# Optimization experiments

Hardware: AMD Instinct MI355X
Metric: run time of the kernel (lower is better)

## Reference

```python
import jax, jax.numpy as jnp
import numpy as np

ALPHA = 1.5
TEMPERATURE = 1.0
N_ITER = 25
N_EMBED = 2048
NUM_EXPERTS = 64
N_TOKENS = 32768


def entmax_bisect(X, alpha=ALPHA, n_iter=N_ITER):
    """Faithful port of entmax.entmax_bisect forward (dim=-1)."""
    d = X.shape[-1]
    inv = 1.0 / (alpha - 1.0)
    Xa = X * (alpha - 1.0)
    max_val = jnp.max(Xa, axis=-1, keepdims=True)
    # _gp(1, alpha) = 1 ; _gp(1/d, alpha) = (1/d)**(1/(alpha-1))
    tau_lo = max_val - 1.0
    tau_hi = max_val - (1.0 / d) ** inv

    def p(tau):
        return jnp.clip(Xa - tau, 0.0, None) ** inv

    f_lo = jnp.sum(p(tau_lo), axis=-1, keepdims=True) - 1.0
    dm0 = tau_hi - tau_lo

    def body(carry, _):
        tau_lo, dm = carry
        dm = dm * 0.5
        tau_m = tau_lo + dm
        p_m = p(tau_m)
        f_m = jnp.sum(p_m, axis=-1, keepdims=True) - 1.0
        mask = (f_m * f_lo) >= 0
        tau_lo = jnp.where(mask, tau_m, tau_lo)
        return (tau_lo, dm), tau_m

    (tau_lo, dm), tau_ms = jax.lax.scan(body, (tau_lo, dm0), None, length=n_iter)
    tau_m_last = tau_ms[-1]  # [..., 1] tau used for the returned p_m in torch loop
    p_m = p(tau_m_last)
    # ensure_sum_one
    p_m = p_m / jnp.sum(p_m, axis=-1, keepdims=True)
    return p_m


def setup_inputs() -> dict:
    key = jax.random.key(0)
    kx, kw, kb = jax.random.split(key, 3)
    x = jax.random.normal(kx, (N_TOKENS, N_EMBED), dtype=jnp.float32)
    # nn.Linear default init: U(-1/sqrt(fan_in), 1/sqrt(fan_in))
    bound = 1.0 / np.sqrt(N_EMBED)
    W = jax.random.uniform(kw, (NUM_EXPERTS, N_EMBED), dtype=jnp.float32, minval=-bound, maxval=bound)
    b = jax.random.uniform(kb, (NUM_EXPERTS,), dtype=jnp.float32, minval=-bound, maxval=bound)
    return {"x": x, "W": W, "b": b}


def reference(x, W, b):
    logits = jnp.einsum("td,ed->te", x, W) + b  # [T, E]
    scaled_logits = logits / TEMPERATURE
    return entmax_bisect(scaled_logits)
```

## Files before the change

kernel.cpp:

```cpp
#include <hip/hip_runtime.h>
#include <hip/hip_bf16.h>
#include <stdint.h>

typedef __bf16 bf16x8 __attribute__((ext_vector_type(8)));
typedef float  f32x4  __attribute__((ext_vector_type(4)));

#define N_EMBED   2048
#define N_EXP     64
#define KCHUNK    64
#define NKC       (N_EMBED / KCHUNK)
#define GCH       16
#define TILEB     16384
#define LGT_STRIDE 68
#define LGT_FLOATS (64 * LGT_STRIDE)

__global__ __launch_bounds__(256) void convert_w_kernel(
        const float* __restrict__ W, uint8_t* __restrict__ wsimg) {
    int tid = blockIdx.x * 256 + threadIdx.x;
    int e   = tid >> 8;
    int d0  = (tid & 255) * 8;
    int kc  = d0 >> 6;
    int dd0 = d0 & 63;
    const float* src = W + e * N_EMBED + d0;
    float4 f0 = *(const float4*)(src);
    float4 f1 = *(const float4*)(src + 4);
    float v[8] = {f0.x, f0.y, f0.z, f0.w, f1.x, f1.y, f1.z, f1.w};
    union { __bf16 h[8]; uint4 u; } hi, lo;
#pragma unroll
    for (int j = 0; j < 8; ++j) {
        float s = 0.5f * v[j];
        __bf16 h = (__bf16)s;
        hi.h[j] = h;
        lo.h[j] = (__bf16)(s - (float)h);
    }
    uint32_t off = (uint32_t)((e * 128 + dd0 * 2) ^ ((e & 7) << 4));
    uint8_t* base = wsimg + (size_t)kc * TILEB + off;
    *(uint4*)(base)        = hi.u;
    *(uint4*)(base + 8192) = lo.u;
}

__device__ __forceinline__ void split8(const float4& p, const float4& q,
                                       bf16x8& h8, bf16x8& l8) {
    float v[8] = {p.x, p.y, p.z, p.w, q.x, q.y, q.z, q.w};
#pragma unroll
    for (int j = 0; j < 8; ++j) {
        __bf16 h = (__bf16)v[j];
        h8[j] = h;
        l8[j] = (__bf16)(v[j] - (float)h);
    }
}

__global__ __launch_bounds__(512, 4) void router_kernel(
        const float* __restrict__ x, const uint8_t* __restrict__ img,
        const float* __restrict__ bias, float* __restrict__ out) {
    __shared__ uint8_t lds[65536];

    const int tid  = threadIdx.x;
    const int wave = tid >> 6;
    const int lane = tid & 63;
    const int l15  = lane & 15;
    const int l4   = lane >> 4;
    const int g    = wave >> 2;
    const int q    = wave & 3;
    const int rowbase = blockIdx.x * 64;
    const float* xrow = x + (size_t)(rowbase + q * 16 + l15) * N_EMBED
                          + g * (GCH * KCHUNK) + l4 * 8;
    uint8_t* lbase = lds + g * 32768;

    uint32_t boff[4][2];
#pragma unroll
    for (int t = 0; t < 4; ++t)
#pragma unroll
        for (int s = 0; s < 2; ++s)
            boff[t][s] = (uint32_t)(((16 * t + l15) * 128 + s * 64 + l4 * 16)
                                    ^ ((l15 & 7) << 4));

    f32x4 acc[4];
#pragma unroll
    for (int t = 0; t < 4; ++t) acc[t] = (f32x4){0.f, 0.f, 0.f, 0.f};

    const int tg  = tid >> 8;
    const int t8  = tid & 255;
    auto STAGE = [&](int i, int buf) {
        const uint8_t* gsrc = img + (size_t)(tg * GCH + i) * TILEB;
        uint8_t* dst = lds + tg * 32768 + buf * TILEB;
#pragma unroll
        for (int j = 0; j < 4; ++j) {
            __builtin_amdgcn_global_load_lds(
                (const __attribute__((address_space(1))) void*)(gsrc + j * 4096 + t8 * 16),
                (__attribute__((address_space(3))) void*)(dst + j * 4096 + t8 * 16),
                16, 0, 0);
        }
    };
    auto LOADA = [&](int i, float4& a0, float4& a1, float4& a2, float4& a3) {
        const float* ap = xrow + i * KCHUNK;
        a0 = *(const float4*)(ap);
        a1 = *(const float4*)(ap + 4);
        a2 = *(const float4*)(ap + 32);
        a3 = *(const float4*)(ap + 36);
    };
    auto MFMAS = [&](int buf, const bf16x8& ah0, const bf16x8& al0,
                     const bf16x8& ah1, const bf16x8& al1) {
        const uint8_t* lb = lbase + (size_t)buf * TILEB;
#pragma unroll
        for (int s = 0; s < 2; ++s) {
            bf16x8 ah = s ? ah1 : ah0;
            bf16x8 al = s ? al1 : al0;
#pragma unroll
            for (int t = 0; t < 4; ++t) {
                bf16x8 bh = *(const bf16x8*)(lb + boff[t][s]);
                bf16x8 bl = *(const bf16x8*)(lb + 8192 + boff[t][s]);
                acc[t] = __builtin_amdgcn_mfma_f32_16x16x32_bf16(ah, bh, acc[t], 0, 0, 0);
                acc[t] = __builtin_amdgcn_mfma_f32_16x16x32_bf16(al, bh, acc[t], 0, 0, 0);
                acc[t] = __builtin_amdgcn_mfma_f32_16x16x32_bf16(ah, bl, acc[t], 0, 0, 0);
            }
        }
    };

    float4 A0, A1, A2, A3, B0, B1, B2, B3;

    STAGE(0, 0);
    __builtin_amdgcn_sched_barrier(0);
    LOADA(0, A0, A1, A2, A3);
    LOADA(1, B0, B1, B2, B3);
    __builtin_amdgcn_sched_barrier(0);
    asm volatile("s_waitcnt vmcnt(8)" ::: "memory");
    __builtin_amdgcn_s_barrier();
    __builtin_amdgcn_sched_barrier(0);

#pragma unroll 1
    for (int i = 0; i < GCH - 2; i += 2) {
        STAGE(i + 1, (i + 1) & 1);
        __builtin_amdgcn_sched_barrier(0);
        {
            bf16x8 ah0, al0, ah1, al1;
            split8(A0, A1, ah0, al0);
            split8(A2, A3, ah1, al1);
            LOADA(i + 2, A0, A1, A2, A3);
            MFMAS(i & 1, ah0, al0, ah1, al1);
        }
        asm volatile("s_waitcnt vmcnt(4) lgkmcnt(0)" ::: "memory");
        __builtin_amdgcn_s_barrier();
        __builtin_amdgcn_sched_barrier(0);

        STAGE(i + 2, i & 1);
        __builtin_amdgcn_sched_barrier(0);
        {
            bf16x8 ah0, al0, ah1, al1;
            split8(B0, B1, ah0, al0);
            split8(B2, B3, ah1, al1);
            LOADA(i + 3, B0, B1, B2, B3);
            MFMAS((i + 1) & 1, ah0, al0, ah1, al1);
        }
        asm volatile("s_waitcnt vmcnt(4) lgkmcnt(0)" ::: "memory");
        __builtin_amdgcn_s_barrier();
        __builtin_amdgcn_sched_barrier(0);
    }

    STAGE(GCH - 1, 1);
    __builtin_amdgcn_sched_barrier(0);
    {
        bf16x8 ah0, al0, ah1, al1;
        split8(A0, A1, ah0, al0);
        split8(A2, A3, ah1, al1);
        MFMAS(0, ah0, al0, ah1, al1);
    }
    asm volatile("s_waitcnt vmcnt(0) lgkmcnt(0)" ::: "memory");
    __builtin_amdgcn_s_barrier();
    __builtin_amdgcn_sched_barrier(0);
    {
        bf16x8 ah0, al0, ah1, al1;
        split8(B0, B1, ah0, al0);
        split8(B2, B3, ah1, al1);
        MFMAS(1, ah0, al0, ah1, al1);
    }

    __syncthreads();
    {
        float* lgt = (float*)lds + g * LGT_FLOATS;
#pragma unroll
        for (int t = 0; t < 4; ++t)
#pragma unroll
            for (int r = 0; r < 4; ++r)
                lgt[(q * 16 + l4 * 4 + r) * LGT_STRIDE + t * 16 + l15] = acc[t][r];
    }
    __syncthreads();

    const float* L0 = (const float*)lds;
    const float* L1 = L0 + LGT_FLOATS;
    float bv0 = 0.5f * bias[l15];
    float bv1 = 0.5f * bias[16 + l15];
    float bv2 = 0.5f * bias[32 + l15];
    float bv3 = 0.5f * bias[48 + l15];

#pragma unroll
    for (int rr = 0; rr < 2; ++rr) {
        int r = g * 2 + rr;
        int row_local = q * 16 + l4 * 4 + r;
        int base = row_local * LGT_STRIDE + l15;
        float v0 = L0[base]      + L1[base]      + bv0;
        float v1 = L0[base + 16] + L1[base + 16] + bv1;
        float v2 = L0[base + 32] + L1[base + 32] + bv2;
        float v3 = L0[base + 48] + L1[base + 48] + bv3;

        float m = fmaxf(fmaxf(v0, v1), fmaxf(v2, v3));
        m = fmaxf(m, __shfl_xor(m, 1, 64));
        m = fmaxf(m, __shfl_xor(m, 2, 64));
        m = fmaxf(m, __shfl_xor(m, 4, 64));
        m = fmaxf(m, __shfl_xor(m, 8, 64));

        float tau_lo = m - 1.0f;
        float tau_hi = m - 0.000244140625f;
        float dm = tau_hi - tau_lo;

        float d0 = fmaxf(v0 - tau_lo, 0.f), d1 = fmaxf(v1 - tau_lo, 0.f);
        float d2 = fmaxf(v2 - tau_lo, 0.f), d3 = fmaxf(v3 - tau_lo, 0.f);
        float s0 = d0 * d0; s0 = fmaf(d1, d1, s0); s0 = fmaf(d2, d2, s0); s0 = fmaf(d3, d3, s0);
        s0 += __shfl_xor(s0, 1, 64);
        s0 += __shfl_xor(s0, 2, 64);
        s0 += __shfl_xor(s0, 4, 64);
        s0 += __shfl_xor(s0, 8, 64);
        const float f_lo = s0 - 1.0f;

        float tau_m = tau_lo, fsum = 1.0f;
#pragma unroll 1
        for (int it = 0; it < 25; ++it) {
            dm *= 0.5f;
            tau_m = tau_lo + dm;
            float e0 = fmaxf(v0 - tau_m, 0.f), e1 = fmaxf(v1 - tau_m, 0.f);
            float e2 = fmaxf(v2 - tau_m, 0.f), e3 = fmaxf(v3 - tau_m, 0.f);
            float s = e0 * e0; s = fmaf(e1, e1, s); s = fmaf(e2, e2, s); s = fmaf(e3, e3, s);
            s += __shfl_xor(s, 1, 64);
            s += __shfl_xor(s, 2, 64);
            s += __shfl_xor(s, 4, 64);
            s += __shfl_xor(s, 8, 64);
            if ((s - 1.0f) * f_lo >= 0.0f) tau_lo = tau_m;
            fsum = s;
        }
        float rinv = 1.0f / fsum;
        float p0 = fmaxf(v0 - tau_m, 0.f); p0 = p0 * p0 * rinv;
        float p1 = fmaxf(v1 - tau_m, 0.f); p1 = p1 * p1 * rinv;
        float p2 = fmaxf(v2 - tau_m, 0.f); p2 = p2 * p2 * rinv;
        float p3 = fmaxf(v3 - tau_m, 0.f); p3 = p3 * p3 * rinv;

        int trow = rowbase + row_local;
        float* op = out + (size_t)trow * N_EXP + l15;
        op[0]  = p0;
        op[16] = p1;
        op[32] = p2;
        op[48] = p3;
    }
}

extern "C" void kernel_launch(void* const* d_in, const int* in_sizes, int n_in,
                              void* d_out, int out_size, void* d_ws, size_t ws_size,
                              hipStream_t stream) {
    (void)n_in; (void)out_size; (void)ws_size;
    const float* x  = (const float*)d_in[0];
    const float* W  = (const float*)d_in[1];
    const float* b  = (const float*)d_in[2];
    float* out      = (float*)d_out;
    uint8_t* wsimg  = (uint8_t*)d_ws;

    const int T = in_sizes[0] / N_EMBED;

    convert_w_kernel<<<dim3(64), dim3(256), 0, stream>>>(W, wsimg);
    router_kernel<<<dim3(T / 64), dim3(512), 0, stream>>>(x, wsimg, b, out);
}
```

Measured before the change: 72.30 us.

## Use single-pass fp16 MFMA instead of split bf16 and restructure entmax epilogue

Replaces the three-MFMA split-bf16 scheme (hi/lo decomposition of x and W) with a single fp16 MFMA per tile, halving the staged weight image and LDS footprint. The entmax epilogue is remapped so each thread handles 8 contiguous experts of one row, using vector LDS loads and float4 stores, with a 3-step instead of 4-step shuffle reduction and one row per wave instead of two unrolled rows. The intent is to cut MFMA work, input conversion ALU, LDS traffic and epilogue overhead. The cost is lower GEMM precision, since fp16 has a short mantissa and x is rounded once with no residual term, which may change bisection outcomes near thresholds.

New measurement: 63.20 us. 1.14x faster.

```diff
diff --git a/kernel.cpp b/kernel.cpp
--- a/kernel.cpp
+++ b/kernel.cpp
@@ -2,15 +2,15 @@
 #include <hip/hip_bf16.h>
 #include <stdint.h>
 
-typedef __bf16 bf16x8 __attribute__((ext_vector_type(8)));
-typedef float  f32x4  __attribute__((ext_vector_type(4)));
+typedef _Float16 half8 __attribute__((ext_vector_type(8)));
+typedef float    f32x4 __attribute__((ext_vector_type(4)));
 
 #define N_EMBED   2048
 #define N_EXP     64
 #define KCHUNK    64
 #define NKC       (N_EMBED / KCHUNK)
 #define GCH       16
-#define TILEB     16384
+#define TILEB     8192
 #define LGT_STRIDE 68
 #define LGT_FLOATS (64 * LGT_STRIDE)
 
@@ -25,35 +25,26 @@
     float4 f0 = *(const float4*)(src);
     float4 f1 = *(const float4*)(src + 4);
     float v[8] = {f0.x, f0.y, f0.z, f0.w, f1.x, f1.y, f1.z, f1.w};
-    union { __bf16 h[8]; uint4 u; } hi, lo;
-#pragma unroll
-    for (int j = 0; j < 8; ++j) {
-        float s = 0.5f * v[j];
-        __bf16 h = (__bf16)s;
-        hi.h[j] = h;
-        lo.h[j] = (__bf16)(s - (float)h);
-    }
+    union { _Float16 h[8]; uint4 u; } hv;
+#pragma unroll
+    for (int j = 0; j < 8; ++j) hv.h[j] = (_Float16)(0.5f * v[j]);
     uint32_t off = (uint32_t)((e * 128 + dd0 * 2) ^ ((e & 7) << 4));
-    uint8_t* base = wsimg + (size_t)kc * TILEB + off;
-    *(uint4*)(base)        = hi.u;
-    *(uint4*)(base + 8192) = lo.u;
-}
-
-__device__ __forceinline__ void split8(const float4& p, const float4& q,
-                                       bf16x8& h8, bf16x8& l8) {
-    float v[8] = {p.x, p.y, p.z, p.w, q.x, q.y, q.z, q.w};
-#pragma unroll
-    for (int j = 0; j < 8; ++j) {
-        __bf16 h = (__bf16)v[j];
-        h8[j] = h;
-        l8[j] = (__bf16)(v[j] - (float)h);
-    }
+    *(uint4*)(wsimg + (size_t)kc * TILEB + off) = hv.u;
+}
+
+__device__ __forceinline__ half8 cvt8(const float4& p, const float4& q) {
+    half8 h;
+    h[0] = (_Float16)p.x; h[1] = (_Float16)p.y;
+    h[2] = (_Float16)p.z; h[3] = (_Float16)p.w;
+    h[4] = (_Float16)q.x; h[5] = (_Float16)q.y;
+    h[6] = (_Float16)q.z; h[7] = (_Float16)q.w;
+    return h;
 }
 
 __global__ __launch_bounds__(512, 4) void router_kernel(
         const float* __restrict__ x, const uint8_t* __restrict__ img,
         const float* __restrict__ bias, float* __restrict__ out) {
-    __shared__ uint8_t lds[65536];
+    __shared__ uint8_t lds[2 * LGT_FLOATS * 4];
 
     const int tid  = threadIdx.x;
     const int wave = tid >> 6;
@@ -65,7 +56,7 @@
     const int rowbase = blockIdx.x * 64;
     const float* xrow = x + (size_t)(rowbase + q * 16 + l15) * N_EMBED
                           + g * (GCH * KCHUNK) + l4 * 8;
-    uint8_t* lbase = lds + g * 32768;
+    uint8_t* lbase = lds + g * 2 * TILEB;
 
     uint32_t boff[4][2];
 #pragma unroll
@@ -83,9 +74,9 @@
     const int t8  = tid & 255;
     auto STAGE = [&](int i, int buf) {
         const uint8_t* gsrc = img + (size_t)(tg * GCH + i) * TILEB;
-        uint8_t* dst = lds + tg * 32768 + buf * TILEB;
-#pragma unroll
-        for (int j = 0; j < 4; ++j) {
+        uint8_t* dst = lds + tg * 2 * TILEB + buf * TILEB;
+#pragma unroll
+        for (int j = 0; j < 2; ++j) {
             __builtin_amdgcn_global_load_lds(
                 (const __attribute__((address_space(1))) void*)(gsrc + j * 4096 + t8 * 16),
                 (__attribute__((address_space(3))) void*)(dst + j * 4096 + t8 * 16),
@@ -99,20 +90,15 @@
         a2 = *(const float4*)(ap + 32);
         a3 = *(const float4*)(ap + 36);
     };
-    auto MFMAS = [&](int buf, const bf16x8& ah0, const bf16x8& al0,
-                     const bf16x8& ah1, const bf16x8& al1) {
+    auto MFMAS = [&](int buf, const half8& a0, const half8& a1) {
         const uint8_t* lb = lbase + (size_t)buf * TILEB;
 #pragma unroll
         for (int s = 0; s < 2; ++s) {
-            bf16x8 ah = s ? ah1 : ah0;
-            bf16x8 al = s ? al1 : al0;
+            half8 ah = s ? a1 : a0;
 #pragma unroll
             for (int t = 0; t < 4; ++t) {
-                bf16x8 bh = *(const bf16x8*)(lb + boff[t][s]);
-                bf16x8 bl = *(const bf16x8*)(lb + 8192 + boff[t][s]);
-                acc[t] = __builtin_amdgcn_mfma_f32_16x16x32_bf16(ah, bh, acc[t], 0, 0, 0);
-                acc[t] = __builtin_amdgcn_mfma_f32_16x16x32_bf16(al, bh, acc[t], 0, 0, 0);
-                acc[t] = __builtin_amdgcn_mfma_f32_16x16x32_bf16(ah, bl, acc[t], 0, 0, 0);
+                half8 bh = *(const half8*)(lb + boff[t][s]);
+                acc[t] = __builtin_amdgcn_mfma_f32_16x16x32_f16(ah, bh, acc[t], 0, 0, 0);
             }
         }
     };
@@ -133,11 +119,10 @@
         STAGE(i + 1, (i + 1) & 1);
         __builtin_amdgcn_sched_barrier(0);
         {
-            bf16x8 ah0, al0, ah1, al1;
-            split8(A0, A1, ah0, al0);
-            split8(A2, A3, ah1, al1);
+            half8 a0 = cvt8(A0, A1);
+            half8 a1 = cvt8(A2, A3);
             LOADA(i + 2, A0, A1, A2, A3);
-            MFMAS(i & 1, ah0, al0, ah1, al1);
+            MFMAS(i & 1, a0, a1);
         }
         asm volatile("s_waitcnt vmcnt(4) lgkmcnt(0)" ::: "memory");
         __builtin_amdgcn_s_barrier();
@@ -146,11 +131,10 @@
         STAGE(i + 2, i & 1);
         __builtin_amdgcn_sched_barrier(0);
         {
-            bf16x8 ah0, al0, ah1, al1;
-            split8(B0, B1, ah0, al0);
-            split8(B2, B3, ah1, al1);
+            half8 a0 = cvt8(B0, B1);
+            half8 a1 = cvt8(B2, B3);
             LOADA(i + 3, B0, B1, B2, B3);
-            MFMAS((i + 1) & 1, ah0, al0, ah1, al1);
+            MFMAS((i + 1) & 1, a0, a1);
         }
         asm volatile("s_waitcnt vmcnt(4) lgkmcnt(0)" ::: "memory");
         __builtin_amdgcn_s_barrier();
@@ -160,19 +144,17 @@
     STAGE(GCH - 1, 1);
     __builtin_amdgcn_sched_barrier(0);
     {
-        bf16x8 ah0, al0, ah1, al1;
-        split8(A0, A1, ah0, al0);
-        split8(A2, A3, ah1, al1);
-        MFMAS(0, ah0, al0, ah1, al1);
+        half8 a0 = cvt8(A0, A1);
+        half8 a1 = cvt8(A2, A3);
+        MFMAS(0, a0, a1);
     }
     asm volatile("s_waitcnt vmcnt(0) lgkmcnt(0)" ::: "memory");
     __builtin_amdgcn_s_barrier();
     __builtin_amdgcn_sched_barrier(0);
     {
-        bf16x8 ah0, al0, ah1, al1;
-        split8(B0, B1, ah0, al0);
-        split8(B2, B3, ah1, al1);
-        MFMAS(1, ah0, al0, ah1, al1);
+        half8 a0 = cvt8(B0, B1);
+        half8 a1 = cvt8(B2, B3);
+        MFMAS(1, a0, a1);
     }
 
     __syncthreads();
@@ -188,68 +170,83 @@
 
     const float* L0 = (const float*)lds;
     const float* L1 = L0 + LGT_FLOATS;
-    float bv0 = 0.5f * bias[l15];
-    float bv1 = 0.5f * bias[16 + l15];
-    float bv2 = 0.5f * bias[32 + l15];
-    float bv3 = 0.5f * bias[48 + l15];
-
-#pragma unroll
-    for (int rr = 0; rr < 2; ++rr) {
-        int r = g * 2 + rr;
-        int row_local = q * 16 + l4 * 4 + r;
-        int base = row_local * LGT_STRIDE + l15;
-        float v0 = L0[base]      + L1[base]      + bv0;
-        float v1 = L0[base + 16] + L1[base + 16] + bv1;
-        float v2 = L0[base + 32] + L1[base + 32] + bv2;
-        float v3 = L0[base + 48] + L1[base + 48] + bv3;
-
-        float m = fmaxf(fmaxf(v0, v1), fmaxf(v2, v3));
-        m = fmaxf(m, __shfl_xor(m, 1, 64));
-        m = fmaxf(m, __shfl_xor(m, 2, 64));
-        m = fmaxf(m, __shfl_xor(m, 4, 64));
-        m = fmaxf(m, __shfl_xor(m, 8, 64));
-
-        float tau_lo = m - 1.0f;
-        float tau_hi = m - 0.000244140625f;
-        float dm = tau_hi - tau_lo;
-
-        float d0 = fmaxf(v0 - tau_lo, 0.f), d1 = fmaxf(v1 - tau_lo, 0.f);
-        float d2 = fmaxf(v2 - tau_lo, 0.f), d3 = fmaxf(v3 - tau_lo, 0.f);
-        float s0 = d0 * d0; s0 = fmaf(d1, d1, s0); s0 = fmaf(d2, d2, s0); s0 = fmaf(d3, d3, s0);
-        s0 += __shfl_xor(s0, 1, 64);
-        s0 += __shfl_xor(s0, 2, 64);
-        s0 += __shfl_xor(s0, 4, 64);
-        s0 += __shfl_xor(s0, 8, 64);
-        const float f_lo = s0 - 1.0f;
-
-        float tau_m = tau_lo, fsum = 1.0f;
+    const int row_local = wave * 8 + (lane >> 3);
+    const int eb = (lane & 7) * 8;
+    const int base = row_local * LGT_STRIDE + eb;
+
+    float v[8];
+    {
+        float4 u0 = *(const float4*)(L0 + base);
+        float4 u1 = *(const float4*)(L0 + base + 4);
+        float4 w0 = *(const float4*)(L1 + base);
+        float4 w1 = *(const float4*)(L1 + base + 4);
+        float4 c0 = *(const float4*)(bias + eb);
+        float4 c1 = *(const float4*)(bias + eb + 4);
+        v[0] = u0.x + w0.x + 0.5f * c0.x;
+        v[1] = u0.y + w0.y + 0.5f * c0.y;
+        v[2] = u0.z + w0.z + 0.5f * c0.z;
+        v[3] = u0.w + w0.w + 0.5f * c0.w;
+        v[4] = u1.x + w1.x + 0.5f * c1.x;
+        v[5] = u1.y + w1.y + 0.5f * c1.y;
+        v[6] = u1.z + w1.z + 0.5f * c1.z;
+        v[7] = u1.w + w1.w + 0.5f * c1.w;
+    }
+
+    float m = v[0];
+#pragma unroll
+    for (int j = 1; j < 8; ++j) m = fmaxf(m, v[j]);
+    m = fmaxf(m, __shfl_xor(m, 1, 64));
+    m = fmaxf(m, __shfl_xor(m, 2, 64));
+    m = fmaxf(m, __shfl_xor(m, 4, 64));
+
+    float tau_lo = m - 1.0f;
+    float tau_hi = m - 0.000244140625f;
+    float dm = tau_hi - tau_lo;
+
+    float s0 = 0.f;
+#pragma unroll
+    for (int j = 0; j < 8; ++j) {
+        float d = fmaxf(v[j] - tau_lo, 0.f);
+        s0 = fmaf(d, d, s0);
+    }
+    s0 += __shfl_xor(s0, 1, 64);
+    s0 += __shfl_xor(s0, 2, 64);
+    s0 += __shfl_xor(s0, 4, 64);
+    const float f_lo = s0 - 1.0f;
+
+    float tau_m = tau_lo, fsum = 1.0f;
 #pragma unroll 1
-        for (int it = 0; it < 25; ++it) {
-            dm *= 0.5f;
-            tau_m = tau_lo + dm;
-            float e0 = fmaxf(v0 - tau_m, 0.f), e1 = fmaxf(v1 - tau_m, 0.f);
-            float e2 = fmaxf(v2 - tau_m, 0.f), e3 = fmaxf(v3 - tau_m, 0.f);
-            float s = e0 * e0; s = fmaf(e1, e1, s); s = fmaf(e2, e2, s); s = fmaf(e3, e3, s);
-            s += __shfl_xor(s, 1, 64);
-            s += __shfl_xor(s, 2, 64);
-            s += __shfl_xor(s, 4, 64);
-            s += __shfl_xor(s, 8, 64);
-            if ((s - 1.0f) * f_lo >= 0.0f) tau_lo = tau_m;
-            fsum = s;
-        }
-        float rinv = 1.0f / fsum;
-        float p0 = fmaxf(v0 - tau_m, 0.f); p0 = p0 * p0 * rinv;
-        float p1 = fmaxf(v1 - tau_m, 0.f); p1 = p1 * p1 * rinv;
-        float p2 = fmaxf(v2 - tau_m, 0.f); p2 = p2 * p2 * rinv;
-        float p3 = fmaxf(v3 - tau_m, 0.f); p3 = p3 * p3 * rinv;
-
-        int trow = rowbase + row_local;
-        float* op = out + (size_t)trow * N_EXP + l15;
-        op[0]  = p0;
-        op[16] = p1;
-        op[32] = p2;
-        op[48] = p3;
-    }
+    for (int it = 0; it < 25; ++it) {
+        dm *= 0.5f;
+        tau_m = tau_lo + dm;
+        float s = 0.f;
+#pragma unroll
+        for (int j = 0; j < 8; ++j) {
+            float d = fmaxf(v[j] - tau_m, 0.f);
+            s = fmaf(d, d, s);
+        }
+        s += __shfl_xor(s, 1, 64);
+        s += __shfl_xor(s, 2, 64);
+        s += __shfl_xor(s, 4, 64);
+        if ((s - 1.0f) * f_lo >= 0.0f) tau_lo = tau_m;
+        fsum = s;
+    }
+    float rinv = 1.0f / fsum;
+    float4 o0, o1;
+    {
+        float d;
+        d = fmaxf(v[0] - tau_m, 0.f); o0.x = d * d * rinv;
+        d = fmaxf(v[1] - tau_m, 0.f); o0.y = d * d * rinv;
+        d = fmaxf(v[2] - tau_m, 0.f); o0.z = d * d * rinv;
+        d = fmaxf(v[3] - tau_m, 0.f); o0.w = d * d * rinv;
+        d = fmaxf(v[4] - tau_m, 0.f); o1.x = d * d * rinv;
+        d = fmaxf(v[5] - tau_m, 0.f); o1.y = d * d * rinv;
+        d = fmaxf(v[6] - tau_m, 0.f); o1.z = d * d * rinv;
+        d = fmaxf(v[7] - tau_m, 0.f); o1.w = d * d * rinv;
+    }
+    float* op = out + (size_t)(rowbase + row_local) * N_EXP + eb;
+    *(float4*)(op)     = o0;
+    *(float4*)(op + 4) = o1;
 }
 
 extern "C" void kernel_launch(void* const* d_in, const int* in_sizes, int n_in,
```
